# Optimization experiments

Measured on AMD Instinct MI355X. Metric: run time of the kernel, lower is better.

The kernel has to match this reference:

```python
import jax, jax.numpy as jnp
import numpy as np

EPS = 1e-8

def setup_inputs() -> dict:
    key = jax.random.key(0)
    k1, k2 = jax.random.split(key)
    x1 = jax.random.normal(k1, (16, 4096, 256), dtype=jnp.float32)
    x2 = jax.random.normal(k2, (16, 4096, 256), dtype=jnp.float32)
    return {"x1": x1, "x2": x2}

def _l2_normalize(x):
    # matches F.normalize / torch norm-with-clamp: x / max(||x||, eps)
    n = jnp.linalg.norm(x, axis=-1, keepdims=True)
    return x / jnp.maximum(n, EPS)

def reference(x1, x2):
    # cosine distance: mean over all segment pairs of (1 - cos_sim)
    # mean_{i,j} (1 - x1n_i . x2n_j) == 1 - (mean_i x1n_i) . (mean_j x2n_j)
    # -- algebraically identical to the original per-batch mm + mean,
    # but avoids materializing the O(n_seg^2) similarity matrix.
    n_batch, embedding_dim = x1.shape[0], x1.shape[-1]
    x1 = x1.reshape(n_batch, -1, embedding_dim)
    x2 = x2.reshape(n_batch, -1, embedding_dim)
    x1n = _l2_normalize(x1)  # (B, S, D)
    x2n = _l2_normalize(x2)
    m1 = x1n.mean(axis=1)    # (B, D)
    m2 = x2n.mean(axis=1)    # (B, D)
    return 1.0 - jnp.einsum('bd,bd->b', m1, m2)  # (B,)
```

## Files before the change

### kernel.cpp

```cpp
#include <hip/hip_runtime.h>


constexpr int D = 256;
constexpr int S = 4096;
constexpr int B = 16;
constexpr int BLOCKS_PER_PAIR = 64;
constexpr int WAVES_PER_BLOCK = 4;
constexpr int WAVES_PER_PAIR  = BLOCKS_PER_PAIR * WAVES_PER_BLOCK;
constexpr int ROWS_PER_WAVE   = S / WAVES_PER_PAIR;
constexpr int NPAIR = 2 * B;
constexpr int NBLK1 = NPAIR * BLOCKS_PER_PAIR;
constexpr float EPS2 = 1e-16f;

template <bool USE_PARTIALS>
__global__ __launch_bounds__(256) void row_norm_sum_kernel(
    const float* __restrict__ x1, const float* __restrict__ x2,
    float* __restrict__ sums )
{
    const int pair = blockIdx.x / BLOCKS_PER_PAIR;
    const int blk  = blockIdx.x % BLOCKS_PER_PAIR;
    const int w    = threadIdx.x >> 6;
    const int lane = threadIdx.x & 63;
    const int wv   = blk * WAVES_PER_BLOCK + w;

    const int batch = pair >> 1;
    const float* __restrict__ src = (pair & 1) ? x2 : x1;
    src += (size_t)batch * S * D;

    float4 acc = make_float4(0.f, 0.f, 0.f, 0.f);

    #pragma unroll
    for (int i = 0; i < ROWS_PER_WAVE; i += 4) {
        float4 v[4];
        float  ss[4];
        #pragma unroll
        for (int k = 0; k < 4; ++k) {
            const int r = wv + (i + k) * WAVES_PER_PAIR;
            v[k] = *(const float4*)(src + (size_t)r * D + lane * 4);
        }
        #pragma unroll
        for (int k = 0; k < 4; ++k)
            ss[k] = v[k].x * v[k].x + v[k].y * v[k].y
                  + v[k].z * v[k].z + v[k].w * v[k].w;
        #pragma unroll
        for (int m = 1; m < 64; m <<= 1) {
            #pragma unroll
            for (int k = 0; k < 4; ++k)
                ss[k] += __shfl_xor(ss[k], m, 64);
        }
        #pragma unroll
        for (int k = 0; k < 4; ++k) {
            const float s = rsqrtf(fmaxf(ss[k], EPS2));
            acc.x += v[k].x * s;
            acc.y += v[k].y * s;
            acc.z += v[k].z * s;
            acc.w += v[k].w * s;
        }
    }

    __shared__ float lds[WAVES_PER_BLOCK][D];
    *(float4*)&lds[w][lane * 4] = acc;
    __syncthreads();

    const int t = threadIdx.x;
    const float val = lds[0][t] + lds[1][t] + lds[2][t] + lds[3][t];
    if (USE_PARTIALS) {
        sums[(size_t)blockIdx.x * D + t] = val;
    } else {
        atomicAdd(&sums[(size_t)pair * D + t], val);
    }
}

__global__ __launch_bounds__(256) void finalize_partials_kernel(
    const float* __restrict__ partials, float* __restrict__ out)
{
    const int b = blockIdx.x;
    const int t = threadIdx.x;
    const int w = t >> 6, lane = t & 63;

    const float* p1 = partials + ((size_t)(2 * b + 0) * BLOCKS_PER_PAIR) * D + t;
    const float* p2 = partials + ((size_t)(2 * b + 1) * BLOCKS_PER_PAIR) * D + t;
    float s1 = 0.f, s2 = 0.f;
    #pragma unroll 8
    for (int k = 0; k < BLOCKS_PER_PAIR; ++k) {
        s1 += p1[(size_t)k * D];
        s2 += p2[(size_t)k * D];
    }
    float d = s1 * s2;
    #pragma unroll
    for (int m = 1; m < 64; m <<= 1) d += __shfl_xor(d, m, 64);

    __shared__ float r[WAVES_PER_BLOCK];
    if (lane == 0) r[w] = d;
    __syncthreads();
    if (t == 0) {
        const float inv = 1.0f / ((float)S * (float)S);
        out[b] = 1.0f - (r[0] + r[1] + r[2] + r[3]) * inv;
    }
}

__global__ __launch_bounds__(64) void finalize_kernel(
    const float* __restrict__ sums, float* __restrict__ out)
{
    const int b = blockIdx.x;
    const int lane = threadIdx.x;
    const float4 a = *(const float4*)(sums + (size_t)(2 * b + 0) * D + lane * 4);
    const float4 c = *(const float4*)(sums + (size_t)(2 * b + 1) * D + lane * 4);
    float d = a.x * c.x + a.y * c.y + a.z * c.z + a.w * c.w;
    #pragma unroll
    for (int m = 1; m < 64; m <<= 1) d += __shfl_xor(d, m, 64);
    if (lane == 0) {
        const float inv = 1.0f / ((float)S * (float)S);
        out[b] = 1.0f - d * inv;
    }
}

extern "C" void kernel_launch(void* const* d_in, const int* in_sizes, int n_in,
                              void* d_out, int out_size, void* d_ws, size_t ws_size,
                              hipStream_t stream) {
    const float* x1 = (const float*)d_in[0];
    const float* x2 = (const float*)d_in[1];
    float* out = (float*)d_out;
    float* ws = (float*)d_ws;

    const size_t partial_bytes = (size_t)NBLK1 * D * sizeof(float);
    if (ws_size >= partial_bytes) {
        row_norm_sum_kernel<true><<<NBLK1, 256, 0, stream>>>(x1, x2, ws);
        finalize_partials_kernel<<<B, 256, 0, stream>>>(ws, out);
    } else {
        hipMemsetAsync(ws, 0, (size_t)NPAIR * D * sizeof(float), stream);
        row_norm_sum_kernel<false><<<NBLK1, 256, 0, stream>>>(x1, x2, ws);
        finalize_kernel<<<B, 64, 0, stream>>>(ws, out);
    }
}
```

Baseline: 146.7 us.

## Process two rows per wave with half-wave DPP norm reduction

Each wave now handles two rows at once, one per 32-lane half. Each lane loads two float4s per row, and all of a lane's loads are issued up front. The per-row squared-norm reduction uses DPP row ops plus a ds_swizzle within 32 lanes instead of a 64-lane shfl_xor butterfly, cutting cross-lane operations that go through LDS. This raises register use and changes the LDS final reduction layout to combine both halves.

```diff
diff --git a/kernel.cpp b/kernel.cpp
--- a/kernel.cpp
+++ b/kernel.cpp
@@ -4,70 +4,87 @@
 constexpr int D = 256;
 constexpr int S = 4096;
 constexpr int B = 16;
-constexpr int BLOCKS_PER_PAIR = 64;
+constexpr int BLOCKS_PER_SEQ = 64;
 constexpr int WAVES_PER_BLOCK = 4;
-constexpr int WAVES_PER_PAIR  = BLOCKS_PER_PAIR * WAVES_PER_BLOCK;
-constexpr int ROWS_PER_WAVE   = S / WAVES_PER_PAIR;
-constexpr int NPAIR = 2 * B;
-constexpr int NBLK1 = NPAIR * BLOCKS_PER_PAIR;
+constexpr int WAVES_PER_SEQ  = BLOCKS_PER_SEQ * WAVES_PER_BLOCK;
+constexpr int PAIRS_PER_WAVE = (S / 2) / WAVES_PER_SEQ;
+constexpr int NSEQ  = 2 * B;
+constexpr int NBLK1 = NSEQ * BLOCKS_PER_SEQ;
 constexpr float EPS2 = 1e-16f;
+
+template <int CTRL>
+__device__ __forceinline__ float dpp_add(float x) {
+    int xi = __builtin_bit_cast(int, x);
+    int yi = __builtin_amdgcn_update_dpp(0, xi, CTRL, 0xf, 0xf, true);
+    return x + __builtin_bit_cast(float, yi);
+}
+
+__device__ __forceinline__ float half_reduce(float x) {
+    x = dpp_add<0xB1>(x);
+    x = dpp_add<0x4E>(x);
+    x = dpp_add<0x141>(x);
+    x = dpp_add<0x140>(x);
+    int xi = __builtin_bit_cast(int, x);
+    int yi = __builtin_amdgcn_ds_swizzle(xi, 0x401F);
+    return x + __builtin_bit_cast(float, yi);
+}
 
 template <bool USE_PARTIALS>
 __global__ __launch_bounds__(256) void row_norm_sum_kernel(
     const float* __restrict__ x1, const float* __restrict__ x2,
     float* __restrict__ sums )
 {
-    const int pair = blockIdx.x / BLOCKS_PER_PAIR;
-    const int blk  = blockIdx.x % BLOCKS_PER_PAIR;
+    const int seq  = blockIdx.x / BLOCKS_PER_SEQ;
+    const int blk  = blockIdx.x % BLOCKS_PER_SEQ;
     const int w    = threadIdx.x >> 6;
     const int lane = threadIdx.x & 63;
+    const int half = lane >> 5;
+    const int l    = lane & 31;
     const int wv   = blk * WAVES_PER_BLOCK + w;
 
-    const int batch = pair >> 1;
-    const float* __restrict__ src = (pair & 1) ? x2 : x1;
-    src += (size_t)batch * S * D;
+    const int batch = seq >> 1;
+    const float* __restrict__ src = (seq & 1) ? x2 : x1;
+    const float* base = src + (size_t)batch * S * D
+                            + (size_t)(2 * wv + half) * D + 4 * l;
 
-    float4 acc = make_float4(0.f, 0.f, 0.f, 0.f);
-
+    float4 vlo[PAIRS_PER_WAVE], vhi[PAIRS_PER_WAVE];
     #pragma unroll
-    for (int i = 0; i < ROWS_PER_WAVE; i += 4) {
-        float4 v[4];
-        float  ss[4];
-        #pragma unroll
-        for (int k = 0; k < 4; ++k) {
-            const int r = wv + (i + k) * WAVES_PER_PAIR;
-            v[k] = *(const float4*)(src + (size_t)r * D + lane * 4);
-        }
-        #pragma unroll
-        for (int k = 0; k < 4; ++k)
-            ss[k] = v[k].x * v[k].x + v[k].y * v[k].y
-                  + v[k].z * v[k].z + v[k].w * v[k].w;
-        #pragma unroll
-        for (int m = 1; m < 64; m <<= 1) {
-            #pragma unroll
-            for (int k = 0; k < 4; ++k)
-                ss[k] += __shfl_xor(ss[k], m, 64);
-        }
-        #pragma unroll
-        for (int k = 0; k < 4; ++k) {
-            const float s = rsqrtf(fmaxf(ss[k], EPS2));
-            acc.x += v[k].x * s;
-            acc.y += v[k].y * s;
-            acc.z += v[k].z * s;
-            acc.w += v[k].w * s;
-        }
+    for (int p = 0; p < PAIRS_PER_WAVE; ++p) {
+        const float* a = base + (size_t)p * (WAVES_PER_SEQ * 2 * D);
+        vlo[p] = *(const float4*)a;
+        vhi[p] = *(const float4*)(a + 128);
     }
 
-    __shared__ float lds[WAVES_PER_BLOCK][D];
-    *(float4*)&lds[w][lane * 4] = acc;
+    float4 acc_lo = make_float4(0.f, 0.f, 0.f, 0.f);
+    float4 acc_hi = make_float4(0.f, 0.f, 0.f, 0.f);
+    #pragma unroll
+    for (int p = 0; p < PAIRS_PER_WAVE; ++p) {
+        float ss = vlo[p].x * vlo[p].x + vlo[p].y * vlo[p].y
+                 + vlo[p].z * vlo[p].z + vlo[p].w * vlo[p].w
+                 + vhi[p].x * vhi[p].x + vhi[p].y * vhi[p].y
+                 + vhi[p].z * vhi[p].z + vhi[p].w * vhi[p].w;
+        ss = half_reduce(ss);
+        const float s = rsqrtf(fmaxf(ss, EPS2));
+        acc_lo.x += vlo[p].x * s;  acc_lo.y += vlo[p].y * s;
+        acc_lo.z += vlo[p].z * s;  acc_lo.w += vlo[p].w * s;
+        acc_hi.x += vhi[p].x * s;  acc_hi.y += vhi[p].y * s;
+        acc_hi.z += vhi[p].z * s;  acc_hi.w += vhi[p].w * s;
+    }
+
+    __shared__ float red[WAVES_PER_BLOCK][2][D];
+    *(float4*)&red[w][half][4 * l]       = acc_lo;
+    *(float4*)&red[w][half][128 + 4 * l] = acc_hi;
     __syncthreads();
 
     const int t = threadIdx.x;
-    const float val = lds[0][t] + lds[1][t] + lds[2][t] + lds[3][t];
+    float val = 0.f;
+    #pragma unroll
+    for (int ww = 0; ww < WAVES_PER_BLOCK; ++ww)
+        val += red[ww][0][t] + red[ww][1][t];
     if (USE_PARTIALS) {
         sums[(size_t)blockIdx.x * D + t] = val;
     } else {
-        atomicAdd(&sums[(size_t)pair * D + t], val);
+        atomicAdd(&sums[(size_t)seq * D + t], val);
     }
 }
 
@@ -78,11 +95,11 @@
     const int t = threadIdx.x;
     const int w = t >> 6, lane = t & 63;
 
-    const float* p1 = partials + ((size_t)(2 * b + 0) * BLOCKS_PER_PAIR) * D + t;
-    const float* p2 = partials + ((size_t)(2 * b + 1) * BLOCKS_PER_PAIR) * D + t;
+    const float* p1 = partials + ((size_t)(2 * b + 0) * BLOCKS_PER_SEQ) * D + t;
+    const float* p2 = partials + ((size_t)(2 * b + 1) * BLOCKS_PER_SEQ) * D + t;
     float s1 = 0.f, s2 = 0.f;
     #pragma unroll 8
-    for (int k = 0; k < BLOCKS_PER_PAIR; ++k) {
+    for (int k = 0; k < BLOCKS_PER_SEQ; ++k) {
         s1 += p1[(size_t)k * D];
         s2 += p2[(size_t)k * D];
     }
@@ -128,7 +145,7 @@
         row_norm_sum_kernel<true><<<NBLK1, 256, 0, stream>>>(x1, x2, ws);
         finalize_partials_kernel<<<B, 256, 0, stream>>>(ws, out);
     } else {
-        hipMemsetAsync(ws, 0, (size_t)NPAIR * D * sizeof(float), stream);
+        hipMemsetAsync(ws, 0, (size_t)NSEQ * D * sizeof(float), stream);
         row_norm_sum_kernel<false><<<NBLK1, 256, 0, stream>>>(x1, x2, ws);
         finalize_kernel<<<B, 64, 0, stream>>>(ws, out);
     }
```

After: 147.8 us. No clear change (+0.8%).
